# Kernel tuning notes

Hardware: AMD Instinct MI355X
Metric: run time of the kernel (lower is better)

## Reference

```python
import jax, jax.numpy as jnp
import numpy as np

EXPAND = 2
KCONV = 4


def _mamba(x, Win, Wconv, bconv, Wx, Wdt, bdt, Alog, Dskip, Wout):
    # x: (B, C, H, W) -> flatten HW to a sequence, run Mamba (S6) block, reshape back
    B, C, H, W = x.shape
    L = H * W
    Di, Kc = Wconv.shape
    R = Wdt.shape[0]
    N = Alog.shape[1]
    xl = x.reshape(B, C, L).transpose(0, 2, 1)            # (B, L, C)
    xz = xl @ Win                                          # (B, L, 2*Di)
    xs, z = xz[..., :Di], xz[..., Di:]
    xt = xs.transpose(0, 2, 1)                             # (B, Di, L)
    xp = jnp.pad(xt, ((0, 0), (0, 0), (Kc - 1, 0)))        # causal depthwise conv1d
    conv = bconv[None, :, None]
    for k in range(Kc):
        conv = conv + Wconv[:, k][None, :, None] * xp[:, :, k:k + L]
    u = jax.nn.silu(conv).transpose(0, 2, 1)               # (B, L, Di)
    dbc = u @ Wx                                           # (B, L, R+2N)
    dt = jax.nn.softplus(dbc[..., :R] @ Wdt + bdt)         # (B, L, Di)
    Bm = dbc[..., R:R + N]                                 # (B, L, N)
    Cm = dbc[..., R + N:]                                  # (B, L, N)
    A = -jnp.exp(Alog)                                     # (Di, N)
    dA = jnp.exp(dt[..., None] * A)                        # (B, L, Di, N)
    dBx = dt[..., None] * Bm[:, :, None, :] * u[..., None] # (B, L, Di, N)

    def step(h, inp):
        a, bx, c = inp
        h = a * h + bx
        return h, jnp.einsum('bdn,bn->bd', h, c)

    h0 = jnp.zeros((B, Di, N), x.dtype)
    _, ys = jax.lax.scan(step, h0, (jnp.swapaxes(dA, 0, 1), jnp.swapaxes(dBx, 0, 1), jnp.swapaxes(Cm, 0, 1)))
    y = jnp.swapaxes(ys, 0, 1) + u * Dskip                 # (B, L, Di)
    y = y * jax.nn.silu(z)
    return (y @ Wout).transpose(0, 2, 1).reshape(B, C, H, W)


def _resize_bilinear(x, oh, ow):
    # F.interpolate(mode='bilinear', align_corners=True)
    B, C, H, W = x.shape
    ys = jnp.linspace(0.0, H - 1.0, oh)
    xs = jnp.linspace(0.0, W - 1.0, ow)
    y0 = jnp.floor(ys).astype(jnp.int32); y1 = jnp.clip(y0 + 1, 0, H - 1); wy = (ys - y0)[:, None]
    x0 = jnp.floor(xs).astype(jnp.int32); x1 = jnp.clip(x0 + 1, 0, W - 1); wx = (xs - x0)[None, :]
    r0 = x[:, :, y0, :]
    r1 = x[:, :, y1, :]
    top = r0[..., x0] * (1 - wx) + r0[..., x1] * wx
    bot = r1[..., x0] * (1 - wx) + r1[..., x1] * wx
    return top * (1 - wy) + bot * wy


def _mamba_params(key, D, N):
    Di = EXPAND * D
    R = max(1, D // 16)
    ks = jax.random.split(key, 6)
    s = 0.02
    Win = s * jax.random.normal(ks[0], (D, 2 * Di), jnp.float32)
    Wconv = s * jax.random.normal(ks[1], (Di, KCONV), jnp.float32)
    bconv = jnp.zeros((Di,), jnp.float32)
    Wx = s * jax.random.normal(ks[2], (Di, R + 2 * N), jnp.float32)
    Wdt = s * jax.random.normal(ks[3], (R, Di), jnp.float32)
    bdt = s * jax.random.normal(ks[4], (Di,), jnp.float32)
    Alog = jnp.tile(jnp.log(jnp.arange(1, N + 1, dtype=jnp.float32))[None, :], (Di, 1))
    Dskip = jnp.ones((Di,), jnp.float32)
    Wout = s * jax.random.normal(ks[5], (Di, D), jnp.float32)
    return Win, Wconv, bconv, Wx, Wdt, bdt, Alog, Dskip, Wout


def setup_inputs() -> dict:
    key = jax.random.key(0)
    C, B, N = 64, 2, 16
    sizes = [48, 24, 12, 6]
    ks = jax.random.split(key, 16)
    inp = {}
    for i, s in enumerate(sizes):
        inp[f'feat{i}'] = jax.random.normal(ks[i], (B, C, s, s), jnp.float32)
    names = ['Win', 'Wconv', 'bconv', 'Wx', 'Wdt', 'bdt', 'Alog', 'D', 'Wout']
    lvl = [_mamba_params(ks[4 + i], C, N) for i in range(4)]
    for j, nm in enumerate(names):
        inp['lvl_' + nm] = jnp.stack([lvl[i][j] for i in range(4)])
    cr = _mamba_params(ks[8], 4 * C, N)
    for j, nm in enumerate(names):
        inp['cr_' + nm] = cr[j]
    inp['proj_W'] = 0.02 * jax.random.normal(ks[9], (C, 4 * C), jnp.float32)  # 1x1 conv weight (out,in)
    inp['proj_b'] = jnp.zeros((C,), jnp.float32)
    inp['bn_g'] = jnp.ones((C,), jnp.float32)
    inp['bn_b'] = jnp.zeros((C,), jnp.float32)
    inp['bn_m'] = 0.1 * jax.random.normal(ks[10], (C,), jnp.float32)
    inp['bn_v'] = jax.random.uniform(ks[11], (C,), jnp.float32, minval=0.5, maxval=1.5)
    inp['target_h'] = 48
    inp['target_w'] = 48
    return inp


def reference(feat0, feat1, feat2, feat3,
              lvl_Win, lvl_Wconv, lvl_bconv, lvl_Wx, lvl_Wdt, lvl_bdt, lvl_Alog, lvl_D, lvl_Wout,
              cr_Win, cr_Wconv, cr_bconv, cr_Wx, cr_Wdt, cr_bdt, cr_Alog, cr_D, cr_Wout,
              proj_W, proj_b, bn_g, bn_b, bn_m, bn_v, target_h, target_w):
    feats = [feat0, feat1, feat2, feat3]
    processed = []
    for i, f in enumerate(feats):
        f = f + _mamba(f, lvl_Win[i], lvl_Wconv[i], lvl_bconv[i], lvl_Wx[i], lvl_Wdt[i],
                       lvl_bdt[i], lvl_Alog[i], lvl_D[i], lvl_Wout[i])
        processed.append(_resize_bilinear(f, target_h, target_w))
    x = jnp.concatenate(processed, axis=1)                 # (B, 4C, th, tw)
    x = x + _mamba(x, cr_Win, cr_Wconv, cr_bconv, cr_Wx, cr_Wdt, cr_bdt, cr_Alog, cr_D, cr_Wout)
    y = jnp.einsum('bchw,oc->bohw', x, proj_W) + proj_b[None, :, None, None]
    scale = (bn_g / jnp.sqrt(bn_v + 1e-5))[None, :, None, None]
    y = (y - bn_m[None, :, None, None]) * scale + bn_b[None, :, None, None]
    return jax.nn.relu(y)
```

## Files before the change

kernel.cpp:

```cpp
#include <hip/hip_runtime.h>
#include <cmath>

#define DEV __device__ __forceinline__

typedef unsigned short u16;
typedef u16 u16x8 __attribute__((ext_vector_type(8)));
typedef u16 u16x4 __attribute__((ext_vector_type(4)));

constexpr int B_ = 2;
constexpr int S4[4]    = {48, 24, 12, 6};
constexpr int L4[4]    = {2304, 576, 144, 36};
constexpr int LOFF4[4] = {0, 2304, 2880, 3024};
constexpr int LTOT = 3060;
constexpr int TOFF4[4] = {0, 144, 180, 189};
constexpr int NTT = 192;
constexpr int NCH4[4]   = {36, 9, 3, 1};
constexpr int CHOFF4[4] = {0, 36, 45, 48};
constexpr int NCHL = 49;
constexpr int NCHC = 36;
constexpr int LC = 2304;
constexpr float LOG2E = 1.44269504088896f;

DEV float siluf(float x) { return x / (1.f + __expf(-x)); }
DEV float softplusf(float x) { return fmaxf(x, 0.f) + log1pf(__expf(-fabsf(x))); }
DEV float b2f(u16 x) { union { float f; unsigned u; } v; v.u = ((unsigned)x) << 16; return v.f; }
DEV u16 f2b(float f) {
  union { float f; unsigned u; } v; v.f = f;
  unsigned r = v.u + 0x7fffu + ((v.u >> 16) & 1u);
  return (u16)(r >> 16);
}

__global__ __launch_bounds__(256) void k_prep(const float* __restrict__ projW,
                                              const float* __restrict__ crWout,
                                              float* __restrict__ Wt,
                                              float* __restrict__ WP) {
  int blk = blockIdx.x;
  if (blk < 64) {
    int i = blk * 256 + threadIdx.x;
    int o = i >> 8, c = i & 255;
    Wt[c * 64 + o] = projW[o * 256 + c];
  } else {
    int i = (blk - 64) * 256 + threadIdx.x;
    int d = i >> 6, o = i & 63;
    float acc = 0.f;
#pragma unroll 4
    for (int c = 0; c < 256; ++c)
      acc = fmaf(crWout[d * 256 + c], projW[o * 256 + c], acc);
    WP[d * 64 + o] = acc;
  }
}

__global__ __launch_bounds__(256) void k_front_lvl(
    const float* __restrict__ f0, const float* __restrict__ f1,
    const float* __restrict__ f2, const float* __restrict__ f3,
    const float* __restrict__ Win,
    const float* __restrict__ Wconv,
    const float* __restrict__ bconv,
    const float* __restrict__ Wx,
    const float* __restrict__ Wdt,
    const float* __restrict__ bdt,
    u16* __restrict__ u_l, u16* __restrict__ dt_l,
    u16* __restrict__ Bm_l, u16* __restrict__ Cm_l, u16* __restrict__ z_l) {
  __shared__ float s_x[64 * 20];
  __shared__ float s_xs[19 * 128];
  __shared__ float s_u[16 * 132];
  __shared__ float s_dbc[16 * 36];
  int bid = blockIdx.x;
  int b = bid / NTT, t = bid - b * NTT;
  int lvl = 0;
  while (lvl < 3 && t >= TOFF4[lvl + 1]) ++lvl;
  int tl = t - TOFF4[lvl];
  int L = L4[lvl], loff = LOFF4[lvl];
  int l0 = tl * 16;
  int nl = min(16, L - l0);
  const float* fx = lvl == 0 ? f0 : lvl == 1 ? f1 : lvl == 2 ? f2 : f3;
  int tid = threadIdx.x;

  for (int i = tid; i < 64 * 20; i += 256) {
    int c = i / 20, r = i - c * 20;
    int l = l0 - 3 + r;
    float v = 0.f;
    if (r < 19 && l >= 0 && l < L) v = fx[(size_t)(b * 64 + c) * L + l];
    s_x[i] = v;
  }
  __syncthreads();
  {
    int j = tid;
    float acc[19];
#pragma unroll
    for (int r = 0; r < 19; ++r) acc[r] = 0.f;
    const float* W = Win + lvl * 64 * 256 + j;
    for (int c = 0; c < 64; ++c) {
      float w = W[c * 256];
#pragma unroll
      for (int r = 0; r < 19; ++r) acc[r] = fmaf(w, s_x[c * 20 + r], acc[r]);
    }
    if (j < 128) {
#pragma unroll
      for (int r = 0; r < 19; ++r) s_xs[r * 128 + j] = acc[r];
    } else {
      int d = j - 128;
      int dti = d >> 4, jj = d & 15;
      for (int r = 3; r < 19; ++r) {
        int l = l0 - 3 + r;
        if (l < l0 + nl)
          z_l[((size_t)(b * 8 + dti) * LTOT + loff + l) * 16 + jj] = f2b(acc[r]);
      }
    }
  }
  __syncthreads();
  for (int i = tid; i < 16 * 128; i += 256) {
    int l = i >> 7, d = i & 127;
    if (l < nl) {
      const float* wc = Wconv + (lvl * 128 + d) * 4;
      float a = bconv[lvl * 128 + d];
#pragma unroll
      for (int k = 0; k < 4; ++k) a = fmaf(wc[k], s_xs[(l + k) * 128 + d], a);
      float uu = siluf(a);
      s_u[l * 132 + d] = uu;
      u_l[((size_t)(b * 8 + (d >> 4)) * LTOT + loff + l0 + l) * 16 + (d & 15)] = f2b(uu);
    }
  }
  __syncthreads();
  for (int i = tid; i < 16 * 36; i += 256) {
    int l = i & 15, jj = i >> 4;
    if (l < nl) {
      const float* wx = Wx + lvl * 128 * 36 + jj;
      float a = 0.f;
      for (int d = 0; d < 128; ++d) a = fmaf(s_u[l * 132 + d], wx[d * 36], a);
      s_dbc[l * 36 + jj] = a;
      if (jj >= 4) {
        int q = jj - 4;
        size_t gb = ((size_t)(b * LTOT) + loff + l0 + l) * 16;
        if (q < 16) Bm_l[gb + q] = f2b(a);
        else        Cm_l[gb + (q - 16)] = f2b(a);
      }
    }
  }
  __syncthreads();
  for (int i = tid; i < 16 * 128; i += 256) {
    int l = i >> 7, d = i & 127;
    if (l < nl) {
      float a = bdt[lvl * 128 + d];
#pragma unroll
      for (int r = 0; r < 4; ++r)
        a = fmaf(s_dbc[l * 36 + r], Wdt[(lvl * 4 + r) * 128 + d], a);
      dt_l[((size_t)(b * 8 + (d >> 4)) * LTOT + loff + l0 + l) * 16 + (d & 15)] =
          f2b(softplusf(a));
    }
  }
}

template <int MODE, int PASSC>
__global__ __launch_bounds__(256) void k_scan(
    const u16* __restrict__ dtb, const u16* __restrict__ ub,
    const u16* __restrict__ Bmb, const u16* __restrict__ Cmb,
    const u16* __restrict__ zb,
    const float* __restrict__ Alog, const float* __restrict__ Dsk,
    float* __restrict__ hloc, float* __restrict__ Ssum,
    const float* __restrict__ hin, u16* __restrict__ yg) {
  constexpr int DI = MODE ? 512 : 128;
  constexpr int NDT = DI / 16;
  constexpr int NCHT = MODE ? NCHC : NCHL;
  constexpr int LT = MODE ? LC : LTOT;
  constexpr int NARR = PASSC ? 5 : 3;
  __shared__ __align__(16) u16 smem[NARR * 1024];
  u16* s_dt = smem;
  u16* s_u = smem + 1024;
  u16* s_B = smem + 2048;
  u16* s_C = PASSC ? smem + 3072 : nullptr;
  u16* s_y = PASSC ? smem + 4096 : nullptr;

  int bid = blockIdx.x;
  int dti = bid % NDT;
  int rem = bid / NDT;
  int gc = rem % NCHT;
  int b = rem / NCHT;
  int lvl = 0, ch = gc, Lq = LC, loff = 0;
  if (MODE == 0) {
    while (lvl < 3 && gc >= CHOFF4[lvl + 1]) ++lvl;
    ch = gc - CHOFF4[lvl];
    Lq = L4[lvl];
    loff = LOFF4[lvl];
  }
  int l0 = ch * 64;
  int len = min(64, Lq - l0);
  int labs0 = loff + l0;
  int tid = threadIdx.x;
  int n = tid & 15, dd = tid >> 4;
  int d = dti * 16 + dd;

  size_t base2 = ((size_t)(b * NDT + dti) * LT + labs0) * 16;
  size_t baseB = ((size_t)b * LT + labs0) * 16;
  {
    int nv = len * 2;
    const u16x8* pdt = (const u16x8*)(dtb + base2);
    const u16x8* pu  = (const u16x8*)(ub + base2);
    const u16x8* pB  = (const u16x8*)(Bmb + baseB);
    u16x8* qdt = (u16x8*)s_dt;
    u16x8* qu  = (u16x8*)s_u;
    u16x8* qB  = (u16x8*)s_B;
    for (int i = tid; i < nv; i += 256) {
      qdt[i] = pdt[i];
      qu[i]  = pu[i];
      qB[i]  = pB[i];
    }
    if (PASSC) {
      const u16x8* pC = (const u16x8*)(Cmb + baseB);
      u16x8* qC = (u16x8*)s_C;
      for (int i = tid; i < nv; i += 256) qC[i] = pC[i];
    }
  }
  __syncthreads();

  int ai = (MODE ? d : lvl * 128 + d);
  float kA2 = -__expf(Alog[ai * 16 + n]) * LOG2E;
  size_t hix = (((size_t)(b * NCHT) + gc) * DI + d) * 16 + n;
  float h = 0.f, ss = 0.f;
  if (PASSC) h = hin[hix];
  float dsk = PASSC ? Dsk[ai] : 0.f;

#pragma unroll 2
  for (int l = 0; l < len; ++l) {
    float dt = b2f(s_dt[l * 16 + dd]);
    float uu = b2f(s_u[l * 16 + dd]);
    float bm = b2f(s_B[l * 16 + n]);
    float dA = exp2f(kA2 * dt);
    h = fmaf(dA, h, dt * uu * bm);
    if (PASSC) {
      float p = h * b2f(s_C[l * 16 + n]);
      p += __shfl_xor(p, 1, 16);
      p += __shfl_xor(p, 2, 16);
      p += __shfl_xor(p, 4, 16);
      p += __shfl_xor(p, 8, 16);
      if (n == 0) s_y[l * 16 + dd] = f2b(fmaf(uu, dsk, p));
    } else {
      ss += dt;
    }
  }
  if (!PASSC) {
    hloc[hix] = h;
    if (n == 0) Ssum[((size_t)(b * NCHT) + gc) * DI + d] = ss;
  } else {
    __syncthreads();
    for (int i = tid; i < len * 16; i += 256) {
      float z = b2f(zb[base2 + i]);
      float gate = z / (1.f + __expf(-z));
      yg[base2 + i] = f2b(b2f(s_y[i]) * gate);
    }
  }
}

__global__ __launch_bounds__(256) void k_combine_lvl(
    const float* __restrict__ Alog, const float* __restrict__ hloc,
    const float* __restrict__ Ssum, float* __restrict__ hin) {
  int i = blockIdx.x * 256 + threadIdx.x;
  int n = i & 15, d = (i >> 4) & 127, lvl = (i >> 11) & 3, b = i >> 13;
  float kA2 = -__expf(Alog[(lvl * 128 + d) * 16 + n]) * LOG2E;
  float h = 0.f;
  int nch = NCH4[lvl];
  for (int ch = 0; ch < nch; ++ch) {
    int gc = CHOFF4[lvl] + ch;
    size_t ix = (((size_t)(b * NCHL) + gc) * 128 + d) * 16 + n;
    hin[ix] = h;
    float S = Ssum[((size_t)(b * NCHL) + gc) * 128 + d];
    h = fmaf(exp2f(kA2 * S), h, hloc[ix]);
  }
}

__global__ __launch_bounds__(256) void k_combine_cr(
    const float* __restrict__ Alog, const float* __restrict__ hloc,
    const float* __restrict__ Ssum, float* __restrict__ hin) {
  int i = blockIdx.x * 256 + threadIdx.x;
  int n = i & 15, d = (i >> 4) & 511, b = i >> 13;
  float kA2 = -__expf(Alog[d * 16 + n]) * LOG2E;
  float h = 0.f;
  for (int ch = 0; ch < NCHC; ++ch) {
    size_t ix = (((size_t)(b * NCHC) + ch) * 512 + d) * 16 + n;
    hin[ix] = h;
    float S = Ssum[((size_t)(b * NCHC) + ch) * 512 + d];
    h = fmaf(exp2f(kA2 * S), h, hloc[ix]);
  }
}

__global__ __launch_bounds__(256) void k_out_lvl(
    const u16* __restrict__ yg_l, const float* __restrict__ Wout,
    const float* __restrict__ f0, const float* __restrict__ f1,
    const float* __restrict__ f2, const float* __restrict__ f3,
    float* __restrict__ fout) {
  __shared__ float s_ygT[128 * 20];
  __shared__ float s_o[16 * 64];
  int bid = blockIdx.x;
  int b = bid / NTT, t = bid - b * NTT;
  int lvl = 0;
  while (lvl < 3 && t >= TOFF4[lvl + 1]) ++lvl;
  int tl = t - TOFF4[lvl];
  int L = L4[lvl], loff = LOFF4[lvl];
  int l0 = tl * 16, nl = min(16, L - l0);
  const float* fx = lvl == 0 ? f0 : lvl == 1 ? f1 : lvl == 2 ? f2 : f3;
  int tid = threadIdx.x;
  for (int i = tid; i < 16 * 128; i += 256) {
    int d = i & 127, l = i >> 7;
    float v = 0.f;
    if (l < nl)
      v = b2f(yg_l[((size_t)(b * 8 + (d >> 4)) * LTOT + loff + l0 + l) * 16 + (d & 15)]);
    s_ygT[d * 20 + l] = v;
  }
  __syncthreads();
  {
    int c = tid & 63, lg = (tid >> 6) * 4;
    float acc[4] = {0.f, 0.f, 0.f, 0.f};
    const float* W = Wout + lvl * 128 * 64 + c;
    for (int dq = 0; dq < 128; ++dq) {
      float w = W[dq * 64];
      float4 yv = *(const float4*)&s_ygT[dq * 20 + lg];
      acc[0] = fmaf(w, yv.x, acc[0]);
      acc[1] = fmaf(w, yv.y, acc[1]);
      acc[2] = fmaf(w, yv.z, acc[2]);
      acc[3] = fmaf(w, yv.w, acc[3]);
    }
#pragma unroll
    for (int a = 0; a < 4; ++a) s_o[(lg + a) * 64 + c] = acc[a];
  }
  __syncthreads();
  for (int i = tid; i < 16 * 64; i += 256) {
    int c = i >> 4, l = i & 15;
    if (l < nl)
      fout[((size_t)(b * 64) + c) * LTOT + loff + l0 + l] =
          s_o[l * 64 + c] + fx[((size_t)(b * 64) + c) * L + l0 + l];
  }
}

__global__ __launch_bounds__(256) void k_resize(const float* __restrict__ fout,
                                                float* __restrict__ xcat) {
  int i = blockIdx.x * 256 + threadIdx.x;
  int hw = i % 2304;
  int rem = i / 2304;
  int ch = rem & 255;
  int b = rem >> 8;
  int oh = hw / 48, ow = hw - oh * 48;
  int lvl = ch >> 6, c = ch & 63;
  int s = S4[lvl];
  const float* base = fout + ((size_t)(b * 64) + c) * LTOT + LOFF4[lvl];
  float scl = (float)(s - 1) * (1.f / 47.f);
  float fy = oh * scl, fxx = ow * scl;
  int y0 = (int)floorf(fy), x0 = (int)floorf(fxx);
  float wy = fy - y0, wx = fxx - x0;
  int y1 = min(y0 + 1, s - 1), x1 = min(x0 + 1, s - 1);
  float v00 = base[y0 * s + x0], v01 = base[y0 * s + x1];
  float v10 = base[y1 * s + x0], v11 = base[y1 * s + x1];
  float top = v00 * (1.f - wx) + v01 * wx;
  float bot = v10 * (1.f - wx) + v11 * wx;
  xcat[i] = top * (1.f - wy) + bot * wy;
}

__global__ __launch_bounds__(256) void k_gemm_in_cr(
    const float* __restrict__ xcat,
    const float* __restrict__ Win,
    u16* __restrict__ xs_c, u16* __restrict__ z_c) {
  __shared__ __align__(16) float s_x[256 * 16];
  __shared__ __align__(16) float s_w[16 * 512];
  int bid = blockIdx.x;
  int jb = bid & 1;
  int rem = bid >> 1;
  int tl = rem % 144, b = rem / 144;
  int l0 = tl * 16;
  int tid = threadIdx.x;
  for (int i = tid; i < 256 * 16; i += 256) {
    int c = i >> 4, l = i & 15;
    s_x[i] = xcat[((size_t)(b * 256) + c) * LC + l0 + l];
  }
  const float* Wb = Win + jb * 512;
  float4 r0, r1, r2, r3, r4, r5, r6, r7;
  auto ldW = [&](int kt, float4& a0, float4& a1, float4& a2, float4& a3,
                 float4& a4, float4& a5, float4& a6, float4& a7) {
    const float* base = Wb + kt * 16 * 1024;
#pragma unroll
    for (int s = 0; s < 8; ++s) {
      int idx = s * 256 + tid;
      int row = idx >> 7, c4 = (idx & 127) << 2;
      float4 v = *(const float4*)&base[row * 1024 + c4];
      if (s == 0) a0 = v; else if (s == 1) a1 = v; else if (s == 2) a2 = v;
      else if (s == 3) a3 = v; else if (s == 4) a4 = v; else if (s == 5) a5 = v;
      else if (s == 6) a6 = v; else a7 = v;
    }
  };
  auto stW = [&](const float4& a0, const float4& a1, const float4& a2,
                 const float4& a3, const float4& a4, const float4& a5,
                 const float4& a6, const float4& a7) {
#pragma unroll
    for (int s = 0; s < 8; ++s) {
      int idx = s * 256 + tid;
      int row = idx >> 7, c4 = (idx & 127) << 2;
      const float4& v = s == 0 ? a0 : s == 1 ? a1 : s == 2 ? a2 : s == 3 ? a3
                      : s == 4 ? a4 : s == 5 ? a5 : s == 6 ? a6 : a7;
      *(float4*)&s_w[row * 512 + c4] = v;
    }
  };

  int j0 = (tid & 63) * 4;
  int lg = (tid >> 6) * 4;
  float acc[4][8];
#pragma unroll
  for (int a = 0; a < 4; ++a)
#pragma unroll
    for (int q = 0; q < 8; ++q) acc[a][q] = 0.f;

  ldW(0, r0, r1, r2, r3, r4, r5, r6, r7);
  stW(r0, r1, r2, r3, r4, r5, r6, r7);
  __syncthreads();
  for (int kt = 0; kt < 16; ++kt) {
    if (kt < 15) ldW(kt + 1, r0, r1, r2, r3, r4, r5, r6, r7);
#pragma unroll
    for (int cc = 0; cc < 16; ++cc) {
      int c = kt * 16 + cc;
      float4 xv = *(const float4*)&s_x[c * 16 + lg];
      float4 w0 = *(const float4*)&s_w[cc * 512 + j0];
      float4 w1 = *(const float4*)&s_w[cc * 512 + j0 + 256];
      float xr[4] = {xv.x, xv.y, xv.z, xv.w};
      float wf[8] = {w0.x, w0.y, w0.z, w0.w, w1.x, w1.y, w1.z, w1.w};
#pragma unroll
      for (int a = 0; a < 4; ++a)
#pragma unroll
        for (int q = 0; q < 8; ++q)
          acc[a][q] = fmaf(xr[a], wf[q], acc[a][q]);
    }
    __syncthreads();
    if (kt < 15) {
      stW(r0, r1, r2, r3, r4, r5, r6, r7);
      __syncthreads();
    }
  }

#pragma unroll
  for (int a = 0; a < 4; ++a) {
    int l = l0 + lg + a;
    u16x4 v0, v1;
    v0.x = f2b(acc[a][0]); v0.y = f2b(acc[a][1]);
    v0.z = f2b(acc[a][2]); v0.w = f2b(acc[a][3]);
    v1.x = f2b(acc[a][4]); v1.y = f2b(acc[a][5]);
    v1.z = f2b(acc[a][6]); v1.w = f2b(acc[a][7]);
    if (jb == 0) {
      *(u16x4*)&xs_c[((size_t)(b * LC) + l) * 512 + j0] = v0;
      *(u16x4*)&xs_c[((size_t)(b * LC) + l) * 512 + j0 + 256] = v1;
    } else {
      int dz0 = j0, dz1 = j0 + 256;
      *(u16x4*)&z_c[((size_t)(b * 32 + (dz0 >> 4)) * LC + l) * 16 + (dz0 & 15)] = v0;
      *(u16x4*)&z_c[((size_t)(b * 32 + (dz1 >> 4)) * LC + l) * 16 + (dz1 & 15)] = v1;
    }
  }
}

__global__ __launch_bounds__(256) void k_mid_cr(
    const u16* __restrict__ xs_c,
    const float* __restrict__ Wconv,
    const float* __restrict__ bconv, const float* __restrict__ Wx,
    const float* __restrict__ Wdt,
    const float* __restrict__ bdt, u16* __restrict__ u_c,
    u16* __restrict__ dt_c, u16* __restrict__ Bm_c, u16* __restrict__ Cm_c) {
  __shared__ __align__(16) u16 s_xs[11 * 512];
  __shared__ float s_u[8 * 516];
  __shared__ float s_dbc[8 * 48];
  int bid = blockIdx.x;
  int b = bid / 288, tl = bid - b * 288;
  int l0 = tl * 8;
  int tid = threadIdx.x;
  for (int i = tid; i < 704; i += 256) {
    int r = i >> 6;
    int l = l0 - 3 + r;
    u16x8 v = {0, 0, 0, 0, 0, 0, 0, 0};
    if (l >= 0)
      v = *(const u16x8*)&xs_c[((size_t)(b * LC) + l) * 512 + (i & 63) * 8];
    *(u16x8*)&s_xs[i * 8] = v;
  }
  __syncthreads();
  for (int i = tid; i < 8 * 512; i += 256) {
    int l = i >> 9, d = i & 511;
    const float* wc = Wconv + d * 4;
    float a = bconv[d];
#pragma unroll
    for (int k = 0; k < 4; ++k) a = fmaf(wc[k], b2f(s_xs[(l + k) * 512 + d]), a);
    float uu = siluf(a);
    s_u[l * 516 + d] = uu;
    u_c[((size_t)(b * 32 + (d >> 4)) * LC + l0 + l) * 16 + (d & 15)] = f2b(uu);
  }
  __syncthreads();
  for (int i = tid; i < 8 * 48; i += 256) {
    int jj = i >> 3, l = i & 7;
    const float* wx = Wx + jj;
    float a = 0.f;
    for (int d = 0; d < 512; ++d) a = fmaf(s_u[l * 516 + d], wx[d * 48], a);
    s_dbc[l * 48 + jj] = a;
    if (jj >= 16) {
      int q = jj - 16;
      size_t gb = ((size_t)(b * LC) + l0 + l) * 16;
      if (q < 16) Bm_c[gb + q] = f2b(a);
      else        Cm_c[gb + (q - 16)] = f2b(a);
    }
  }
  __syncthreads();
  for (int i = tid; i < 8 * 512; i += 256) {
    int l = i >> 9, d = i & 511;
    float a = bdt[d];
#pragma unroll
    for (int r = 0; r < 16; ++r)
      a = fmaf(s_dbc[l * 48 + r], Wdt[r * 512 + d], a);
    dt_c[((size_t)(b * 32 + (d >> 4)) * LC + l0 + l) * 16 + (d & 15)] =
        f2b(softplusf(a));
  }
}

__global__ __launch_bounds__(256) void k_final(
    const float* __restrict__ xcat, const u16* __restrict__ yg_c,
    const float* __restrict__ Wt, const float* __restrict__ WP,
    const float* __restrict__ pb, const float* __restrict__ bng,
    const float* __restrict__ bnb, const float* __restrict__ bnm,
    const float* __restrict__ bnv, float* __restrict__ out) {
  __shared__ float s_xc[256 * 16];
  __shared__ float s_ygT[512 * 16];
  __shared__ float s_w[32 * 64];
  int bid = blockIdx.x;
  int b = bid / 144, tl = bid - b * 144;
  int l0 = tl * 16;
  int tid = threadIdx.x;
  for (int i = tid; i < 256 * 16; i += 256) {
    int c = i >> 4, l = i & 15;
    s_xc[i] = xcat[((size_t)(b * 256) + c) * LC + l0 + l];
  }
  for (int i = tid; i < 16 * 512; i += 256) {
    int d = i >> 4, l = i & 15;
    s_ygT[i] =
        b2f(yg_c[((size_t)(b * 32 + (d >> 4)) * LC + l0 + l) * 16 + (d & 15)]);
  }
  int o = tid & 63, lg = (tid >> 6) * 4;
  float acc[4] = {0.f, 0.f, 0.f, 0.f};
  float4 r0, r1;
  auto ldT = [&](const float* W, int kt, float4& a0, float4& a1) {
#pragma unroll
    for (int s = 0; s < 2; ++s) {
      int idx = s * 256 + tid;
      int row = idx >> 4, c4 = (idx & 15) << 2;
      float4 v = *(const float4*)&W[(kt * 32 + row) * 64 + c4];
      if (s == 0) a0 = v; else a1 = v;
    }
  };
  auto stT = [&](const float4& a0, const float4& a1) {
#pragma unroll
    for (int s = 0; s < 2; ++s) {
      int idx = s * 256 + tid;
      int row = idx >> 4, c4 = (idx & 15) << 2;
      *(float4*)&s_w[row * 64 + c4] = (s == 0) ? a0 : a1;
    }
  };
  ldT(Wt, 0, r0, r1);
  __syncthreads();
  stT(r0, r1);
  __syncthreads();
  for (int kt = 0; kt < 8; ++kt) {
    if (kt < 7) ldT(Wt, kt + 1, r0, r1);
    else ldT(WP, 0, r0, r1);
#pragma unroll
    for (int cc = 0; cc < 32; ++cc) {
      float w = s_w[cc * 64 + o];
      float4 xv = *(const float4*)&s_xc[(kt * 32 + cc) * 16 + lg];
      acc[0] = fmaf(w, xv.x, acc[0]);
      acc[1] = fmaf(w, xv.y, acc[1]);
      acc[2] = fmaf(w, xv.z, acc[2]);
      acc[3] = fmaf(w, xv.w, acc[3]);
    }
    __syncthreads();
    stT(r0, r1);
    __syncthreads();
  }
  for (int kt = 0; kt < 16; ++kt) {
    if (kt < 15) ldT(WP, kt + 1, r0, r1);
#pragma unroll
    for (int cc = 0; cc < 32; ++cc) {
      float w = s_w[cc * 64 + o];
      float4 yv = *(const float4*)&s_ygT[(kt * 32 + cc) * 16 + lg];
      acc[0] = fmaf(w, yv.x, acc[0]);
      acc[1] = fmaf(w, yv.y, acc[1]);
      acc[2] = fmaf(w, yv.z, acc[2]);
      acc[3] = fmaf(w, yv.w, acc[3]);
    }
    __syncthreads();
    if (kt < 15) {
      stT(r0, r1);
      __syncthreads();
    }
  }
  float bias = pb[o], m = bnm[o], g = bng[o], v = bnv[o], bb = bnb[o];
  float scl = g * (1.f / sqrtf(v + 1e-5f));
  float4 r;
  r.x = fmaxf((acc[0] + bias - m) * scl + bb, 0.f);
  r.y = fmaxf((acc[1] + bias - m) * scl + bb, 0.f);
  r.z = fmaxf((acc[2] + bias - m) * scl + bb, 0.f);
  r.w = fmaxf((acc[3] + bias - m) * scl + bb, 0.f);
  *(float4*)&out[((size_t)(b * 64) + o) * LC + l0 + lg] = r;
}

extern "C" void kernel_launch(void* const* d_in, const int* in_sizes, int n_in,
                              void* d_out, int out_size, void* d_ws,
                              size_t ws_size, hipStream_t stream) {
  (void)in_sizes; (void)n_in; (void)out_size; (void)ws_size;
  const float* f0 = (const float*)d_in[0];
  const float* f1 = (const float*)d_in[1];
  const float* f2 = (const float*)d_in[2];
  const float* f3 = (const float*)d_in[3];
  const float* lWin   = (const float*)d_in[4];
  const float* lWconv = (const float*)d_in[5];
  const float* lbconv = (const float*)d_in[6];
  const float* lWx    = (const float*)d_in[7];
  const float* lWdt   = (const float*)d_in[8];
  const float* lbdt   = (const float*)d_in[9];
  const float* lAlog  = (const float*)d_in[10];
  const float* lD     = (const float*)d_in[11];
  const float* lWout  = (const float*)d_in[12];
  const float* cWin   = (const float*)d_in[13];
  const float* cWconv = (const float*)d_in[14];
  const float* cbconv = (const float*)d_in[15];
  const float* cWx    = (const float*)d_in[16];
  const float* cWdt   = (const float*)d_in[17];
  const float* cbdt   = (const float*)d_in[18];
  const float* cAlog  = (const float*)d_in[19];
  const float* cD     = (const float*)d_in[20];
  const float* cWout  = (const float*)d_in[21];
  const float* projW  = (const float*)d_in[22];
  const float* projb  = (const float*)d_in[23];
  const float* bng    = (const float*)d_in[24];
  const float* bnb    = (const float*)d_in[25];
  const float* bnm    = (const float*)d_in[26];
  const float* bnv    = (const float*)d_in[27];
  float* out = (float*)d_out;

  float* ws = (float*)d_ws;
  size_t off = 0;
  auto allocf = [&](size_t n) { float* p = ws + off; off += (n + 7) & ~(size_t)7; return p; };
  auto allocb = [&](size_t n) { u16* p = (u16*)(ws + off); off += ((n + 1) / 2 + 7) & ~(size_t)7; return p; };

  float* Wt     = allocf(256 * 64);
  float* WP     = allocf(512 * 64);
  float* fout   = allocf((size_t)B_ * 64 * LTOT);
  float* xcat   = allocf((size_t)B_ * 256 * LC);
  float* hloc_l = allocf((size_t)B_ * NCHL * 128 * 16);
  float* S_l    = allocf((size_t)B_ * NCHL * 128);
  float* hin_l  = allocf((size_t)B_ * NCHL * 128 * 16);
  float* hloc_c = allocf((size_t)B_ * NCHC * 512 * 16);
  float* S_c    = allocf((size_t)B_ * NCHC * 512);
  float* hin_c  = allocf((size_t)B_ * NCHC * 512 * 16);

  u16* u_l2  = allocb((size_t)B_ * 8 * LTOT * 16);
  u16* dt_l2 = allocb((size_t)B_ * 8 * LTOT * 16);
  u16* z_l2  = allocb((size_t)B_ * 8 * LTOT * 16);
  u16* yg_l2 = allocb((size_t)B_ * 8 * LTOT * 16);
  u16* Bm_l2 = allocb((size_t)B_ * LTOT * 16);
  u16* Cm_l2 = allocb((size_t)B_ * LTOT * 16);
  u16* xs_c2 = allocb((size_t)B_ * LC * 512);
  u16* u_c2  = allocb((size_t)B_ * 32 * LC * 16);
  u16* dt_c2 = allocb((size_t)B_ * 32 * LC * 16);
  u16* z_c2  = allocb((size_t)B_ * 32 * LC * 16);
  u16* yg_c2 = allocb((size_t)B_ * 32 * LC * 16);
  u16* Bm_c2 = allocb((size_t)B_ * LC * 16);
  u16* Cm_c2 = allocb((size_t)B_ * LC * 16);

  k_prep<<<192, 256, 0, stream>>>(projW, cWout, Wt, WP);

  k_front_lvl<<<B_ * NTT, 256, 0, stream>>>(f0, f1, f2, f3, lWin, lWconv,
                                            lbconv, lWx, lWdt, lbdt, u_l2,
                                            dt_l2, Bm_l2, Cm_l2, z_l2);

  k_scan<0, 0><<<B_ * 8 * NCHL, 256, 0, stream>>>(
      dt_l2, u_l2, Bm_l2, Cm_l2, nullptr, lAlog, lD, hloc_l, S_l, nullptr,
      nullptr);
  k_combine_lvl<<<64, 256, 0, stream>>>(lAlog, hloc_l, S_l, hin_l);
  k_scan<0, 1><<<B_ * 8 * NCHL, 256, 0, stream>>>(
      dt_l2, u_l2, Bm_l2, Cm_l2, z_l2, lAlog, lD, nullptr, nullptr, hin_l,
      yg_l2);

  k_out_lvl<<<B_ * NTT, 256, 0, stream>>>(yg_l2, lWout, f0, f1, f2, f3, fout);
  k_resize<<<(B_ * 256 * LC) / 256, 256, 0, stream>>>(fout, xcat);

  k_gemm_in_cr<<<B_ * 144 * 2, 256, 0, stream>>>(xcat, cWin, xs_c2, z_c2);
  k_mid_cr<<<B_ * 288, 256, 0, stream>>>(xs_c2, cWconv, cbconv, cWx, cWdt,
                                         cbdt, u_c2, dt_c2, Bm_c2, Cm_c2);

  k_scan<1, 0><<<B_ * 32 * NCHC, 256, 0, stream>>>(
      dt_c2, u_c2, Bm_c2, Cm_c2, nullptr, cAlog, cD, hloc_c, S_c, nullptr,
      nullptr);
  k_combine_cr<<<64, 256, 0, stream>>>(cAlog, hloc_c, S_c, hin_c);
  k_scan<1, 1><<<B_ * 32 * NCHC, 256, 0, stream>>>(
      dt_c2, u_c2, Bm_c2, Cm_c2, z_c2, cAlog, cD, nullptr, nullptr, hin_c,
      yg_c2);

  k_final<<<B_ * 144, 256, 0, stream>>>(xcat, yg_c2, Wt, WP, projb, bng, bnb,
                                        bnm, bnv, out);
}
```

Baseline: 390.8 us.

## Use bf16 MFMA for cross-level input projection with transposed bf16 operands

Replaces the fp32 FMA GEMM for the cross-level Win projection with a bf16 MFMA 16x16x32 kernel. The resize kernel now writes a token-major layout in both fp32 and bf16, and Win is pre-transposed to bf16 in the prep kernel. Wx is also pre-transposed so the mid kernel can use vectorized float4 loads, and the final kernel uses 8-token tiles with twice as many blocks. The cost is extra bf16 rounding of the input activations, an additional output buffer written by resize, and scalar scattered stores in the MFMA epilogue.

```diff
diff --git a/kernel.cpp b/kernel.cpp
--- a/kernel.cpp
+++ b/kernel.cpp
@@ -6,6 +6,8 @@
 typedef unsigned short u16;
 typedef u16 u16x8 __attribute__((ext_vector_type(8)));
 typedef u16 u16x4 __attribute__((ext_vector_type(4)));
+typedef short bf16x8 __attribute__((ext_vector_type(8)));
+typedef float f32x4 __attribute__((ext_vector_type(4)));
 
 constexpr int B_ = 2;
 constexpr int S4[4]    = {48, 24, 12, 6};
@@ -30,23 +32,43 @@
   return (u16)(r >> 16);
 }
 
-__global__ __launch_bounds__(256) void k_prep(const float* __restrict__ projW,
-                                              const float* __restrict__ crWout,
-                                              float* __restrict__ Wt,
-                                              float* __restrict__ WP) {
+__global__ __launch_bounds__(256) void k_prep(
+    const float* __restrict__ projW, const float* __restrict__ crWout,
+    const float* __restrict__ cWin, const float* __restrict__ cWx,
+    float* __restrict__ Wt, float* __restrict__ WP,
+    u16* __restrict__ WinT, float* __restrict__ WxT) {
+  __shared__ float sm[64 * 65];
   int blk = blockIdx.x;
+  int tid = threadIdx.x;
   if (blk < 64) {
-    int i = blk * 256 + threadIdx.x;
+    int i = blk * 256 + tid;
     int o = i >> 8, c = i & 255;
     Wt[c * 64 + o] = projW[o * 256 + c];
-  } else {
-    int i = (blk - 64) * 256 + threadIdx.x;
+  } else if (blk < 192) {
+    int i = (blk - 64) * 256 + tid;
     int d = i >> 6, o = i & 63;
     float acc = 0.f;
 #pragma unroll 4
     for (int c = 0; c < 256; ++c)
       acc = fmaf(crWout[d * 256 + c], projW[o * 256 + c], acc);
     WP[d * 64 + o] = acc;
+  } else if (blk < 256) {
+    int t = blk - 192;
+    int ct = t & 3, nt = t >> 2;
+    int c0 = ct * 64, n0 = nt * 64;
+    for (int i = tid; i < 4096; i += 256) {
+      int cc = i >> 6, nn = i & 63;
+      sm[cc * 65 + nn] = cWin[(size_t)(c0 + cc) * 1024 + n0 + nn];
+    }
+    __syncthreads();
+    for (int i = tid; i < 4096; i += 256) {
+      int nn = i >> 6, cc = i & 63;
+      WinT[(size_t)(n0 + nn) * 256 + c0 + cc] = f2b(sm[cc * 65 + nn]);
+    }
+  } else {
+    int i = (blk - 256) * 256 + tid;
+    int d = i & 511, j = i >> 9;
+    WxT[j * 512 + d] = cWx[d * 48 + j];
   }
 }
 
@@ -332,12 +354,13 @@
 }
 
 __global__ __launch_bounds__(256) void k_resize(const float* __restrict__ fout,
-                                                float* __restrict__ xcat) {
+                                                float* __restrict__ xTf,
+                                                u16* __restrict__ xTb) {
   int i = blockIdx.x * 256 + threadIdx.x;
-  int hw = i % 2304;
-  int rem = i / 2304;
-  int ch = rem & 255;
-  int b = rem >> 8;
+  int ch = i & 255;
+  int rem = i >> 8;
+  int hw = rem % 2304;
+  int b = rem / 2304;
   int oh = hw / 48, ow = hw - oh * 48;
   int lvl = ch >> 6, c = ch & 63;
   int s = S4[lvl];
@@ -351,102 +374,108 @@
   float v10 = base[y1 * s + x0], v11 = base[y1 * s + x1];
   float top = v00 * (1.f - wx) + v01 * wx;
   float bot = v10 * (1.f - wx) + v11 * wx;
-  xcat[i] = top * (1.f - wy) + bot * wy;
-}
-
-__global__ __launch_bounds__(256) void k_gemm_in_cr(
-    const float* __restrict__ xcat,
-    const float* __restrict__ Win,
+  float v = top * (1.f - wy) + bot * wy;
+  xTf[i] = v;
+  xTb[i] = f2b(v);
+}
+
+__global__ __launch_bounds__(256) void k_gemm_mfma(
+    const u16* __restrict__ xT,
+    const u16* __restrict__ WT,
     u16* __restrict__ xs_c, u16* __restrict__ z_c) {
-  __shared__ __align__(16) float s_x[256 * 16];
-  __shared__ __align__(16) float s_w[16 * 512];
+  __shared__ __align__(16) u16 s_a[64 * 72];
+  __shared__ __align__(16) u16 s_b[128 * 72];
   int bid = blockIdx.x;
-  int jb = bid & 1;
-  int rem = bid >> 1;
-  int tl = rem % 144, b = rem / 144;
-  int l0 = tl * 16;
+  int nj = bid & 7, bm = bid >> 3;
   int tid = threadIdx.x;
-  for (int i = tid; i < 256 * 16; i += 256) {
-    int c = i >> 4, l = i & 15;
-    s_x[i] = xcat[((size_t)(b * 256) + c) * LC + l0 + l];
-  }
-  const float* Wb = Win + jb * 512;
-  float4 r0, r1, r2, r3, r4, r5, r6, r7;
-  auto ldW = [&](int kt, float4& a0, float4& a1, float4& a2, float4& a3,
-                 float4& a4, float4& a5, float4& a6, float4& a7) {
-    const float* base = Wb + kt * 16 * 1024;
-#pragma unroll
-    for (int s = 0; s < 8; ++s) {
-      int idx = s * 256 + tid;
-      int row = idx >> 7, c4 = (idx & 127) << 2;
-      float4 v = *(const float4*)&base[row * 1024 + c4];
-      if (s == 0) a0 = v; else if (s == 1) a1 = v; else if (s == 2) a2 = v;
-      else if (s == 3) a3 = v; else if (s == 4) a4 = v; else if (s == 5) a5 = v;
-      else if (s == 6) a6 = v; else a7 = v;
+  int lane = tid & 63, w = tid >> 6;
+  int wm = (w & 1) * 32, wn = (w >> 1) * 64;
+  const int m_base = bm * 64;
+  const int n_base = nj * 128;
+
+  f32x4 acc[2][4];
+#pragma unroll
+  for (int mi = 0; mi < 2; ++mi)
+#pragma unroll
+    for (int ni = 0; ni < 4; ++ni) acc[mi][ni] = {0.f, 0.f, 0.f, 0.f};
+
+  u16x8 ra0, ra1, rb0, rb1, rb2, rb3;
+  auto ld = [&](int c0) {
+#pragma unroll
+    for (int s = 0; s < 2; ++s) {
+      int v = s * 256 + tid;
+      int row = v >> 3, kc = (v & 7) * 8;
+      u16x8 t = *(const u16x8*)&xT[(size_t)(m_base + row) * 256 + c0 + kc];
+      if (s == 0) ra0 = t; else ra1 = t;
+    }
+#pragma unroll
+    for (int s = 0; s < 4; ++s) {
+      int v = s * 256 + tid;
+      int row = v >> 3, kc = (v & 7) * 8;
+      u16x8 t = *(const u16x8*)&WT[(size_t)(n_base + row) * 256 + c0 + kc];
+      if (s == 0) rb0 = t; else if (s == 1) rb1 = t;
+      else if (s == 2) rb2 = t; else rb3 = t;
     }
   };
-  auto stW = [&](const float4& a0, const float4& a1, const float4& a2,
-                 const float4& a3, const float4& a4, const float4& a5,
-                 const float4& a6, const float4& a7) {
-#pragma unroll
-    for (int s = 0; s < 8; ++s) {
-      int idx = s * 256 + tid;
-      int row = idx >> 7, c4 = (idx & 127) << 2;
-      const float4& v = s == 0 ? a0 : s == 1 ? a1 : s == 2 ? a2 : s == 3 ? a3
-                      : s == 4 ? a4 : s == 5 ? a5 : s == 6 ? a6 : a7;
-      *(float4*)&s_w[row * 512 + c4] = v;
+  auto st = [&]() {
+#pragma unroll
+    for (int s = 0; s < 2; ++s) {
+      int v = s * 256 + tid;
+      int row = v >> 3, kc = (v & 7) * 8;
+      *(u16x8*)&s_a[row * 72 + kc] = (s == 0) ? ra0 : ra1;
+    }
+#pragma unroll
+    for (int s = 0; s < 4; ++s) {
+      int v = s * 256 + tid;
+      int row = v >> 3, kc = (v & 7) * 8;
+      const u16x8& t = (s == 0) ? rb0 : (s == 1) ? rb1 : (s == 2) ? rb2 : rb3;
+      *(u16x8*)&s_b[row * 72 + kc] = t;
     }
   };
-
-  int j0 = (tid & 63) * 4;
-  int lg = (tid >> 6) * 4;
-  float acc[4][8];
-#pragma unroll
-  for (int a = 0; a < 4; ++a)
-#pragma unroll
-    for (int q = 0; q < 8; ++q) acc[a][q] = 0.f;
-
-  ldW(0, r0, r1, r2, r3, r4, r5, r6, r7);
-  stW(r0, r1, r2, r3, r4, r5, r6, r7);
-  __syncthreads();
-  for (int kt = 0; kt < 16; ++kt) {
-    if (kt < 15) ldW(kt + 1, r0, r1, r2, r3, r4, r5, r6, r7);
-#pragma unroll
-    for (int cc = 0; cc < 16; ++cc) {
-      int c = kt * 16 + cc;
-      float4 xv = *(const float4*)&s_x[c * 16 + lg];
-      float4 w0 = *(const float4*)&s_w[cc * 512 + j0];
-      float4 w1 = *(const float4*)&s_w[cc * 512 + j0 + 256];
-      float xr[4] = {xv.x, xv.y, xv.z, xv.w};
-      float wf[8] = {w0.x, w0.y, w0.z, w0.w, w1.x, w1.y, w1.z, w1.w};
-#pragma unroll
-      for (int a = 0; a < 4; ++a)
-#pragma unroll
-        for (int q = 0; q < 8; ++q)
-          acc[a][q] = fmaf(xr[a], wf[q], acc[a][q]);
-    }
+  ld(0);
+  int mlane = lane & 15, kg = (lane >> 4) * 8;
+  for (int kt = 0; kt < 4; ++kt) {
+    st();
     __syncthreads();
-    if (kt < 15) {
-      stW(r0, r1, r2, r3, r4, r5, r6, r7);
-      __syncthreads();
-    }
-  }
-
-#pragma unroll
-  for (int a = 0; a < 4; ++a) {
-    int l = l0 + lg + a;
-    u16x4 v0, v1;
-    v0.x = f2b(acc[a][0]); v0.y = f2b(acc[a][1]);
-    v0.z = f2b(acc[a][2]); v0.w = f2b(acc[a][3]);
-    v1.x = f2b(acc[a][4]); v1.y = f2b(acc[a][5]);
-    v1.z = f2b(acc[a][6]); v1.w = f2b(acc[a][7]);
-    if (jb == 0) {
-      *(u16x4*)&xs_c[((size_t)(b * LC) + l) * 512 + j0] = v0;
-      *(u16x4*)&xs_c[((size_t)(b * LC) + l) * 512 + j0 + 256] = v1;
-    } else {
-      int dz0 = j0, dz1 = j0 + 256;
-      *(u16x4*)&z_c[((size_t)(b * 32 + (dz0 >> 4)) * LC + l) * 16 + (dz0 & 15)] = v0;
-      *(u16x4*)&z_c[((size_t)(b * 32 + (dz1 >> 4)) * LC + l) * 16 + (dz1 & 15)] = v1;
+    if (kt < 3) ld((kt + 1) * 64);
+#pragma unroll
+    for (int kk = 0; kk < 2; ++kk) {
+      int k0 = kk * 32 + kg;
+      bf16x8 af[2], bfr[4];
+#pragma unroll
+      for (int mi = 0; mi < 2; ++mi)
+        af[mi] = *(const bf16x8*)&s_a[(wm + mi * 16 + mlane) * 72 + k0];
+#pragma unroll
+      for (int ni = 0; ni < 4; ++ni)
+        bfr[ni] = *(const bf16x8*)&s_b[(wn + ni * 16 + mlane) * 72 + k0];
+#pragma unroll
+      for (int mi = 0; mi < 2; ++mi)
+#pragma unroll
+        for (int ni = 0; ni < 4; ++ni)
+          acc[mi][ni] = __builtin_amdgcn_mfma_f32_16x16x32_bf16(
+              af[mi], bfr[ni], acc[mi][ni], 0, 0, 0);
+    }
+    __syncthreads();
+  }
+  int rgrp = (lane >> 4) * 4;
+#pragma unroll
+  for (int mi = 0; mi < 2; ++mi) {
+#pragma unroll
+    for (int ni = 0; ni < 4; ++ni) {
+      int n = n_base + wn + ni * 16 + mlane;
+#pragma unroll
+      for (int r = 0; r < 4; ++r) {
+        int gm = m_base + wm + mi * 16 + rgrp + r;
+        int b = gm >= 2304;
+        int l = gm - b * 2304;
+        u16 v = f2b(acc[mi][ni][r]);
+        if (n < 512) {
+          xs_c[((size_t)(b * LC) + l) * 512 + n] = v;
+        } else {
+          int dz = n - 512;
+          z_c[((size_t)(b * 32 + (dz >> 4)) * LC + l) * 16 + (dz & 15)] = v;
+        }
+      }
     }
   }
 }
@@ -454,12 +483,13 @@
 __global__ __launch_bounds__(256) void k_mid_cr(
     const u16* __restrict__ xs_c,
     const float* __restrict__ Wconv,
-    const float* __restrict__ bconv, const float* __restrict__ Wx,
+    const float* __restrict__ bconv,
+    const float* __restrict__ WxT,
     const float* __restrict__ Wdt,
     const float* __restrict__ bdt, u16* __restrict__ u_c,
     u16* __restrict__ dt_c, u16* __restrict__ Bm_c, u16* __restrict__ Cm_c) {
   __shared__ __align__(16) u16 s_xs[11 * 512];
-  __shared__ float s_u[8 * 516];
+  __shared__ __align__(16) float s_u[8 * 516];
   __shared__ float s_dbc[8 * 48];
   int bid = blockIdx.x;
   int b = bid / 288, tl = bid - b * 288;
@@ -487,9 +517,17 @@
   __syncthreads();
   for (int i = tid; i < 8 * 48; i += 256) {
     int jj = i >> 3, l = i & 7;
-    const float* wx = Wx + jj;
+    const float* wx = WxT + jj * 512;
     float a = 0.f;
-    for (int d = 0; d < 512; ++d) a = fmaf(s_u[l * 516 + d], wx[d * 48], a);
+#pragma unroll 4
+    for (int d = 0; d < 512; d += 4) {
+      float4 w4 = *(const float4*)&wx[d];
+      float4 u4 = *(const float4*)&s_u[l * 516 + d];
+      a = fmaf(w4.x, u4.x, a);
+      a = fmaf(w4.y, u4.y, a);
+      a = fmaf(w4.z, u4.z, a);
+      a = fmaf(w4.w, u4.w, a);
+    }
     s_dbc[l * 48 + jj] = a;
     if (jj >= 16) {
       int q = jj - 16;
@@ -511,29 +549,29 @@
 }
 
 __global__ __launch_bounds__(256) void k_final(
-    const float* __restrict__ xcat, const u16* __restrict__ yg_c,
+    const float* __restrict__ xTf, const u16* __restrict__ yg_c,
     const float* __restrict__ Wt, const float* __restrict__ WP,
     const float* __restrict__ pb, const float* __restrict__ bng,
     const float* __restrict__ bnb, const float* __restrict__ bnm,
     const float* __restrict__ bnv, float* __restrict__ out) {
-  __shared__ float s_xc[256 * 16];
-  __shared__ float s_ygT[512 * 16];
+  __shared__ float s_xc[256 * 8];
+  __shared__ float s_yg[512 * 8];
   __shared__ float s_w[32 * 64];
   int bid = blockIdx.x;
-  int b = bid / 144, tl = bid - b * 144;
-  int l0 = tl * 16;
+  int b = bid / 288, tl = bid - b * 288;
+  int l0 = tl * 8;
   int tid = threadIdx.x;
-  for (int i = tid; i < 256 * 16; i += 256) {
-    int c = i >> 4, l = i & 15;
-    s_xc[i] = xcat[((size_t)(b * 256) + c) * LC + l0 + l];
-  }
-  for (int i = tid; i < 16 * 512; i += 256) {
-    int d = i >> 4, l = i & 15;
-    s_ygT[i] =
-        b2f(yg_c[((size_t)(b * 32 + (d >> 4)) * LC + l0 + l) * 16 + (d & 15)]);
-  }
-  int o = tid & 63, lg = (tid >> 6) * 4;
-  float acc[4] = {0.f, 0.f, 0.f, 0.f};
+  for (int i = tid; i < 2048; i += 256) {
+    int c = i & 255, l = i >> 8;
+    s_xc[c * 8 + l] = xTf[((size_t)(b * 2304) + l0 + l) * 256 + c];
+  }
+  for (int i = tid; i < 4096; i += 256) {
+    int j = i & 15, l = (i >> 4) & 7, dt = i >> 7;
+    s_yg[(dt * 16 + j) * 8 + l] =
+        b2f(yg_c[((size_t)(b * 32 + dt) * LC + l0 + l) * 16 + j]);
+  }
+  int o = tid & 63, lg = (tid >> 6) * 2;
+  float acc0 = 0.f, acc1 = 0.f;
   float4 r0, r1;
   auto ldT = [&](const float* W, int kt, float4& a0, float4& a1) {
 #pragma unroll
@@ -562,11 +600,9 @@
 #pragma unroll
     for (int cc = 0; cc < 32; ++cc) {
       float w = s_w[cc * 64 + o];
-      float4 xv = *(const float4*)&s_xc[(kt * 32 + cc) * 16 + lg];
-      acc[0] = fmaf(w, xv.x, acc[0]);
-      acc[1] = fmaf(w, xv.y, acc[1]);
-      acc[2] = fmaf(w, xv.z, acc[2]);
-      acc[3] = fmaf(w, xv.w, acc[3]);
+      float2 xv = *(const float2*)&s_xc[(kt * 32 + cc) * 8 + lg];
+      acc0 = fmaf(w, xv.x, acc0);
+      acc1 = fmaf(w, xv.y, acc1);
     }
     __syncthreads();
     stT(r0, r1);
@@ -577,11 +613,9 @@
 #pragma unroll
     for (int cc = 0; cc < 32; ++cc) {
       float w = s_w[cc * 64 + o];
-      float4 yv = *(const float4*)&s_ygT[(kt * 32 + cc) * 16 + lg];
-      acc[0] = fmaf(w, yv.x, acc[0]);
-      acc[1] = fmaf(w, yv.y, acc[1]);
-      acc[2] = fmaf(w, yv.z, acc[2]);
-      acc[3] = fmaf(w, yv.w, acc[3]);
+      float2 yv = *(const float2*)&s_yg[(kt * 32 + cc) * 8 + lg];
+      acc0 = fmaf(w, yv.x, acc0);
+      acc1 = fmaf(w, yv.y, acc1);
     }
     __syncthreads();
     if (kt < 15) {
@@ -591,12 +625,10 @@
   }
   float bias = pb[o], m = bnm[o], g = bng[o], v = bnv[o], bb = bnb[o];
   float scl = g * (1.f / sqrtf(v + 1e-5f));
-  float4 r;
-  r.x = fmaxf((acc[0] + bias - m) * scl + bb, 0.f);
-  r.y = fmaxf((acc[1] + bias - m) * scl + bb, 0.f);
-  r.z = fmaxf((acc[2] + bias - m) * scl + bb, 0.f);
-  r.w = fmaxf((acc[3] + bias - m) * scl + bb, 0.f);
-  *(float4*)&out[((size_t)(b * 64) + o) * LC + l0 + lg] = r;
+  float2 r;
+  r.x = fmaxf((acc0 + bias - m) * scl + bb, 0.f);
+  r.y = fmaxf((acc1 + bias - m) * scl + bb, 0.f);
+  *(float2*)&out[((size_t)(b * 64) + o) * LC + l0 + lg] = r;
 }
 
 extern "C" void kernel_launch(void* const* d_in, const int* in_sizes, int n_in,
@@ -640,8 +672,9 @@
 
   float* Wt     = allocf(256 * 64);
   float* WP     = allocf(512 * 64);
+  float* WxT    = allocf(48 * 512);
   float* fout   = allocf((size_t)B_ * 64 * LTOT);
-  float* xcat   = allocf((size_t)B_ * 256 * LC);
+  float* xTf    = allocf((size_t)B_ * LC * 256);
   float* hloc_l = allocf((size_t)B_ * NCHL * 128 * 16);
   float* S_l    = allocf((size_t)B_ * NCHL * 128);
   float* hin_l  = allocf((size_t)B_ * NCHL * 128 * 16);
@@ -649,6 +682,8 @@
   float* S_c    = allocf((size_t)B_ * NCHC * 512);
   float* hin_c  = allocf((size_t)B_ * NCHC * 512 * 16);
 
+  u16* WinT  = allocb(1024 * 256);
+  u16* xTb   = allocb((size_t)B_ * LC * 256);
   u16* u_l2  = allocb((size_t)B_ * 8 * LTOT * 16);
   u16* dt_l2 = allocb((size_t)B_ * 8 * LTOT * 16);
   u16* z_l2  = allocb((size_t)B_ * 8 * LTOT * 16);
@@ -663,7 +698,7 @@
   u16* Bm_c2 = allocb((size_t)B_ * LC * 16);
   u16* Cm_c2 = allocb((size_t)B_ * LC * 16);
 
-  k_prep<<<192, 256, 0, stream>>>(projW, cWout, Wt, WP);
+  k_prep<<<352, 256, 0, stream>>>(projW, cWout, cWin, cWx, Wt, WP, WinT, WxT);
 
   k_front_lvl<<<B_ * NTT, 256, 0, stream>>>(f0, f1, f2, f3, lWin, lWconv,
                                             lbconv, lWx, lWdt, lbdt, u_l2,
@@ -678,10 +713,10 @@
       yg_l2);
 
   k_out_lvl<<<B_ * NTT, 256, 0, stream>>>(yg_l2, lWout, f0, f1, f2, f3, fout);
-  k_resize<<<(B_ * 256 * LC) / 256, 256, 0, stream>>>(fout, xcat);
-
-  k_gemm_in_cr<<<B_ * 144 * 2, 256, 0, stream>>>(xcat, cWin, xs_c2, z_c2);
-  k_mid_cr<<<B_ * 288, 256, 0, stream>>>(xs_c2, cWconv, cbconv, cWx, cWdt,
+  k_resize<<<(B_ * 256 * LC) / 256, 256, 0, stream>>>(fout, xTf, xTb);
+
+  k_gemm_mfma<<<72 * 8, 256, 0, stream>>>(xTb, WinT, xs_c2, z_c2);
+  k_mid_cr<<<B_ * 288, 256, 0, stream>>>(xs_c2, cWconv, cbconv, WxT, cWdt,
                                          cbdt, u_c2, dt_c2, Bm_c2, Cm_c2);
 
   k_scan<1, 0><<<B_ * 32 * NCHC, 256, 0, stream>>>(
@@ -692,6 +727,6 @@
       dt_c2, u_c2, Bm_c2, Cm_c2, z_c2, cAlog, cD, nullptr, nullptr, hin_c,
       yg_c2);
 
-  k_final<<<B_ * 144, 256, 0, stream>>>(xcat, yg_c2, Wt, WP, projb, bng, bnb,
+  k_final<<<B_ * 288, 256, 0, stream>>>(xTf, yg_c2, Wt, WP, projb, bng, bnb,
                                         bnm, bnv, out);
 }
```

New measurement: 357.6 us. -8.5%, faster.
